# Optimization experiments

Measured on AMD Instinct MI355X. Metric: run time of the kernel, lower is better.

The kernel has to match this reference:

```python
import jax, jax.numpy as jnp
import numpy as np

NUM_PHONEMES = 512
D = 128  # embed_dim == hidden_channels == out_channels (forced by residuals)
N = 50000
E = 500000
PAD_ID = 0
LN_EPS = 1e-5


def setup_inputs() -> dict:
    key = jax.random.key(0)
    ks = jax.random.split(key, 12)
    node_ids = jax.random.randint(ks[0], (N,), 0, NUM_PHONEMES)
    edge_index = jax.random.randint(ks[1], (2, E), 0, N)
    emb = jax.random.normal(ks[2], (NUM_PHONEMES, D), jnp.float32) * 0.05
    emb = emb.at[PAD_ID].set(0.0)  # padding_idx row zeroed
    W1 = jax.random.normal(ks[3], (D, D), jnp.float32) * (1.0 / np.sqrt(D))
    b1 = jnp.zeros((D,), jnp.float32)
    W2 = jax.random.normal(ks[4], (D, D), jnp.float32) * (1.0 / np.sqrt(D))
    b2 = jnp.zeros((D,), jnp.float32)
    g1 = jnp.ones((D,), jnp.float32)
    beta1 = jnp.zeros((D,), jnp.float32)
    g2 = jnp.ones((D,), jnp.float32)
    beta2 = jnp.zeros((D,), jnp.float32)
    return {"node_ids": node_ids, "edge_index": edge_index, "emb": emb,
            "W1": W1, "b1": b1, "W2": W2, "b2": b2,
            "g1": g1, "beta1": beta1, "g2": g2, "beta2": beta2}


def _gcn_conv(x, src, dst, W, b):
    """PyG GCNConv with add_self_loops=True, normalize=True.
    out = D^{-1/2} (A + I) D^{-1/2} (x W) + b, deg computed after self-loops."""
    n = x.shape[0]
    loop = jnp.arange(n, dtype=src.dtype)
    src_f = jnp.concatenate([src, loop])  # [E+N]
    dst_f = jnp.concatenate([dst, loop])
    deg = jax.ops.segment_sum(jnp.ones_like(dst_f, dtype=x.dtype), dst_f,
                              num_segments=n)  # >=1 due to self-loops
    dis = jax.lax.rsqrt(deg)
    norm = dis[src_f] * dis[dst_f]  # [E+N]
    h = x @ W  # [N, D_out]
    msg = h[src_f] * norm[:, None]  # [E+N, D_out] gather (memory-bound)
    out = jax.ops.segment_sum(msg, dst_f, num_segments=n)  # scatter-add
    return out + b


def _layernorm(x, g, b):
    mu = jnp.mean(x, axis=-1, keepdims=True)
    var = jnp.mean(jnp.square(x - mu), axis=-1, keepdims=True)
    return (x - mu) * jax.lax.rsqrt(var + LN_EPS) * g + b


def reference(node_ids, edge_index, emb, W1, b1, W2, b2, g1, beta1, g2, beta2):
    src, dst = edge_index[0], edge_index[1]
    x = emb[node_ids]  # embedding lookup [N, D]
    h1 = _gcn_conv(x, src, dst, W1, b1)
    x = _layernorm(x + h1, g1, beta1)  # dropout is identity in eval mode
    h2 = _gcn_conv(x, src, dst, W2, b2)
    x = _layernorm(x + h2, g2, beta2)
    return x
```

## Files before the change

kernel.cpp:

```cpp
#include <hip/hip_runtime.h>

#define DD 128
#define CAP 32
#define SPILL_MAX 4096

typedef __attribute__((ext_vector_type(8))) short short8;
typedef __attribute__((ext_vector_type(4))) float float4v;

static __device__ __forceinline__ unsigned short f2bf(float x) {
    unsigned u = __builtin_bit_cast(unsigned, x);
    u += 0x7fffu + ((u >> 16) & 1u);
    return (unsigned short)(u >> 16);
}
static __device__ __forceinline__ float bflo(unsigned u) {
    return __builtin_bit_cast(float, u << 16);
}
static __device__ __forceinline__ float bfhi(unsigned u) {
    return __builtin_bit_cast(float, u & 0xffff0000u);
}

__global__ __launch_bounds__(256) void k_init(const float* __restrict__ emb,
                                              const float* __restrict__ W1,
                                              const float* __restrict__ W2,
                                              unsigned* __restrict__ embW1b,
                                              unsigned short* __restrict__ Wb,
                                              const int* __restrict__ src,
                                              const int* __restrict__ dst,
                                              const int* __restrict__ node_ids,
                                              int* __restrict__ cursor,
                                              unsigned* __restrict__ recs,
                                              int* __restrict__ spillCnt,
                                              int* __restrict__ spill_d,
                                              int* __restrict__ spill_r, int E) {
    int blk = blockIdx.x;
    if (blk < 128) {
        int w = threadIdx.x >> 6;
        int t = threadIdx.x & 63;
        int p = blk * 4 + w;
        int c0 = t * 2, c1 = t * 2 + 1;
        float s0 = 0.f, s1 = 0.f;
#pragma unroll 8
        for (int k = 0; k < DD; k++) {
            float e = emb[p * DD + k];
            s0 += e * W1[k * DD + c0];
            s1 += e * W1[k * DD + c1];
        }
        embW1b[p * 64 + t] = (unsigned)f2bf(s0) | ((unsigned)f2bf(s1) << 16);
    } else if (blk < 136) {
        int t = (blk - 128) * 256 + threadIdx.x;
        int nt = t >> 8, ks = (t >> 6) & 3, lane = t & 63;
        int n = nt * 16 + (lane & 15);
        int kbase = ks * 32 + (lane >> 4) * 8;
        unsigned short* o = Wb + (size_t)t * 8;
#pragma unroll
        for (int j = 0; j < 8; j++)
            o[j] = f2bf(W2[(kbase + j) * DD + n]);
    } else {
        int base = ((blk - 136) * 256 + threadIdx.x) * 4;
        if (base >= E) return;
#pragma unroll
        for (int u = 0; u < 4; u++) {
            int e = base + u;
            if (e >= E) break;
            int s = src[e], d = dst[e];
            unsigned rec = (unsigned)s | ((unsigned)node_ids[s] << 16);
            int pos = atomicAdd(&cursor[d], 1);
            if (pos < CAP) {
                recs[(size_t)d * CAP + pos] = rec;
            } else {
                int sp = atomicAdd(spillCnt, 1);
                if (sp < SPILL_MAX) { spill_d[sp] = d; spill_r[sp] = (int)rec; }
            }
        }
    }
}

__global__ __launch_bounds__(256) void k_node1(const int* __restrict__ cursor,
                                               const unsigned* __restrict__ recs,
                                               const int* __restrict__ node_ids,
                                               const float* __restrict__ emb,
                                               const unsigned* __restrict__ embW1b,
                                               const int* __restrict__ spillCnt,
                                               const int* __restrict__ spill_d,
                                               const int* __restrict__ spill_r,
                                               const float* __restrict__ b1,
                                               const float* __restrict__ g1,
                                               const float* __restrict__ beta1,
                                               unsigned* __restrict__ x1b, int N) {
    int gid = blockIdx.x * blockDim.x + threadIdx.x;
    int wave = gid >> 6;
    int lane = threadIdx.x & 63;
    int qtr = lane >> 4;
    int l = lane & 15;
    int qbase = lane & 48;
    int i = wave * 4 + qtr;
    if (i >= N) return;
    int dg = cursor[i];
    int r0 = i * CAP;
    int r1 = r0 + ((dg < CAP) ? dg : CAP);
    int c = l * 8;
    float a0 = 0.f, a1 = 0.f, a2 = 0.f, a3 = 0.f, a4 = 0.f, a5 = 0.f, a6 = 0.f, a7 = 0.f;
    for (int j0 = r0; j0 < r1; j0 += 16) {
        int pidx = j0 + l;
        unsigned rv = recs[(pidx < r1) ? pidx : (r1 - 1)];
        int lim = r1 - j0;
#pragma unroll
        for (int q = 0; q < 16; q++) {
            unsigned rec = __shfl(rv, qbase + q, 64);
            int s = rec & 0xFFFFu;
            float n = rsqrtf((float)cursor[s] + 1.0f);
            n = (q < lim) ? n : 0.f;
            uint4 a = *(const uint4*)(embW1b + ((rec >> 16) & 511u) * 64 + l * 4);
            a0 += bflo(a.x) * n; a1 += bfhi(a.x) * n;
            a2 += bflo(a.y) * n; a3 += bfhi(a.y) * n;
            a4 += bflo(a.z) * n; a5 += bfhi(a.z) * n;
            a6 += bflo(a.w) * n; a7 += bfhi(a.w) * n;
        }
    }
    if (dg > CAP) {
        int sc = *spillCnt; if (sc > SPILL_MAX) sc = SPILL_MAX;
        for (int j = 0; j < sc; j++) {
            if (spill_d[j] == i) {
                unsigned rec = (unsigned)spill_r[j];
                int s = rec & 0xFFFFu;
                float n = rsqrtf((float)cursor[s] + 1.0f);
                uint4 a = *(const uint4*)(embW1b + ((rec >> 16) & 511u) * 64 + l * 4);
                a0 += bflo(a.x) * n; a1 += bfhi(a.x) * n;
                a2 += bflo(a.y) * n; a3 += bfhi(a.y) * n;
                a4 += bflo(a.z) * n; a5 += bfhi(a.z) * n;
                a6 += bflo(a.w) * n; a7 += bfhi(a.w) * n;
            }
        }
    }
    float di = rsqrtf((float)dg + 1.0f);
    int pid = node_ids[i];
    float4 ev0 = *(const float4*)(emb + (size_t)pid * DD + c);
    float4 ev1 = *(const float4*)(emb + (size_t)pid * DD + c + 4);
    uint4 hw = *(const uint4*)(embW1b + pid * 64 + l * 4);
    float4 bb0 = *(const float4*)(b1 + c);
    float4 bb1 = *(const float4*)(b1 + c + 4);
    float v0 = ev0.x + di * (a0 + di * bflo(hw.x)) + bb0.x;
    float v1 = ev0.y + di * (a1 + di * bfhi(hw.x)) + bb0.y;
    float v2 = ev0.z + di * (a2 + di * bflo(hw.y)) + bb0.z;
    float v3 = ev0.w + di * (a3 + di * bfhi(hw.y)) + bb0.w;
    float v4 = ev1.x + di * (a4 + di * bflo(hw.z)) + bb1.x;
    float v5 = ev1.y + di * (a5 + di * bfhi(hw.z)) + bb1.y;
    float v6 = ev1.z + di * (a6 + di * bflo(hw.w)) + bb1.z;
    float v7 = ev1.w + di * (a7 + di * bfhi(hw.w)) + bb1.w;
    float sum = v0 + v1 + v2 + v3 + v4 + v5 + v6 + v7;
#pragma unroll
    for (int o = 8; o >= 1; o >>= 1) sum += __shfl_xor(sum, o, 64);
    float mu = sum * (1.f / DD);
    float d0 = v0 - mu, d1 = v1 - mu, d2 = v2 - mu, d3 = v3 - mu;
    float d4 = v4 - mu, d5 = v5 - mu, d6 = v6 - mu, d7 = v7 - mu;
    float ss = d0 * d0 + d1 * d1 + d2 * d2 + d3 * d3 + d4 * d4 + d5 * d5 + d6 * d6 + d7 * d7;
#pragma unroll
    for (int o = 8; o >= 1; o >>= 1) ss += __shfl_xor(ss, o, 64);
    float r = rsqrtf(ss * (1.f / DD) + 1e-5f);
    float4 gg0 = *(const float4*)(g1 + c);
    float4 gg1 = *(const float4*)(g1 + c + 4);
    float4 be0 = *(const float4*)(beta1 + c);
    float4 be1 = *(const float4*)(beta1 + c + 4);
    float o0 = d0 * r * gg0.x + be0.x;
    float o1 = d1 * r * gg0.y + be0.y;
    float o2 = d2 * r * gg0.z + be0.z;
    float o3 = d3 * r * gg0.w + be0.w;
    float o4 = d4 * r * gg1.x + be1.x;
    float o5 = d5 * r * gg1.y + be1.y;
    float o6 = d6 * r * gg1.z + be1.z;
    float o7 = d7 * r * gg1.w + be1.w;
    uint4 pk;
    pk.x = (unsigned)f2bf(o0) | ((unsigned)f2bf(o1) << 16);
    pk.y = (unsigned)f2bf(o2) | ((unsigned)f2bf(o3) << 16);
    pk.z = (unsigned)f2bf(o4) | ((unsigned)f2bf(o5) << 16);
    pk.w = (unsigned)f2bf(o6) | ((unsigned)f2bf(o7) << 16);
    *(uint4*)(x1b + (size_t)i * 64 + l * 4) = pk;
}

__global__ __launch_bounds__(256) void k_node2(const int* __restrict__ cursor,
                                               const unsigned* __restrict__ recs,
                                               const unsigned* __restrict__ x1b,
                                               const int* __restrict__ spillCnt,
                                               const int* __restrict__ spill_d,
                                               const int* __restrict__ spill_r,
                                               const float* __restrict__ b2,
                                               const float* __restrict__ g2,
                                               const float* __restrict__ beta2,
                                               const unsigned short* __restrict__ Wb,
                                               float* __restrict__ out, int N) {
    __shared__ unsigned tileA[16 * 68];
    __shared__ float tileH[16 * 132];
    int wv = threadIdx.x >> 6;
    int lane = threadIdx.x & 63;
    int qtr = lane >> 4;
    int l = lane & 15;
    int qbase = lane & 48;
    int base16 = blockIdx.x * 16;
    int i = base16 + wv * 4 + qtr;
    uint4 xv = make_uint4(0, 0, 0, 0);
    float bb[8] = {0, 0, 0, 0, 0, 0, 0, 0};
    int c = l * 8;
    if (i < N) {
        int dg = cursor[i];
        int r0 = i * CAP;
        int r1 = r0 + ((dg < CAP) ? dg : CAP);
        float a0 = 0.f, a1 = 0.f, a2 = 0.f, a3 = 0.f, a4 = 0.f, a5 = 0.f, a6 = 0.f, a7 = 0.f;
        for (int j0 = r0; j0 < r1; j0 += 16) {
            int pidx = j0 + l;
            unsigned rv = recs[(pidx < r1) ? pidx : (r1 - 1)];
            int lim = r1 - j0;
#pragma unroll
            for (int q = 0; q < 16; q++) {
                unsigned s = __shfl(rv, qbase + q, 64) & 0xFFFFu;
                float n = rsqrtf((float)cursor[s] + 1.0f);
                n = (q < lim) ? n : 0.f;
                uint4 a = *(const uint4*)(x1b + (size_t)s * 64 + l * 4);
                a0 += bflo(a.x) * n; a1 += bfhi(a.x) * n;
                a2 += bflo(a.y) * n; a3 += bfhi(a.y) * n;
                a4 += bflo(a.z) * n; a5 += bfhi(a.z) * n;
                a6 += bflo(a.w) * n; a7 += bfhi(a.w) * n;
            }
        }
        if (dg > CAP) {
            int sc = *spillCnt; if (sc > SPILL_MAX) sc = SPILL_MAX;
            for (int j = 0; j < sc; j++) {
                if (spill_d[j] == i) {
                    unsigned s = (unsigned)spill_r[j] & 0xFFFFu;
                    float n = rsqrtf((float)cursor[s] + 1.0f);
                    uint4 a = *(const uint4*)(x1b + (size_t)s * 64 + l * 4);
                    a0 += bflo(a.x) * n; a1 += bfhi(a.x) * n;
                    a2 += bflo(a.y) * n; a3 += bfhi(a.y) * n;
                    a4 += bflo(a.z) * n; a5 += bfhi(a.z) * n;
                    a6 += bflo(a.w) * n; a7 += bfhi(a.w) * n;
                }
            }
        }
        float di = rsqrtf((float)dg + 1.0f);
        xv = *(const uint4*)(x1b + (size_t)i * 64 + l * 4);
        float z0 = a0 + di * bflo(xv.x);
        float z1 = a1 + di * bfhi(xv.x);
        float z2 = a2 + di * bflo(xv.y);
        float z3 = a3 + di * bfhi(xv.y);
        float z4 = a4 + di * bflo(xv.z);
        float z5 = a5 + di * bfhi(xv.z);
        float z6 = a6 + di * bflo(xv.w);
        float z7 = a7 + di * bfhi(xv.w);
        uint4 pk;
        pk.x = (unsigned)f2bf(z0) | ((unsigned)f2bf(z1) << 16);
        pk.y = (unsigned)f2bf(z2) | ((unsigned)f2bf(z3) << 16);
        pk.z = (unsigned)f2bf(z4) | ((unsigned)f2bf(z5) << 16);
        pk.w = (unsigned)f2bf(z6) | ((unsigned)f2bf(z7) << 16);
        *(uint4*)(tileA + (wv * 4 + qtr) * 68 + l * 4) = pk;
        float4 t0 = *(const float4*)(b2 + c);
        float4 t1 = *(const float4*)(b2 + c + 4);
        bb[0] = t0.x; bb[1] = t0.y; bb[2] = t0.z; bb[3] = t0.w;
        bb[4] = t1.x; bb[5] = t1.y; bb[6] = t1.z; bb[7] = t1.w;
    }
    __syncthreads();
    {
        int m = l;
        int quad = qtr;
        short8 afr[4];
        const char* tb = (const char*)tileA;
#pragma unroll
        for (int ks = 0; ks < 4; ks++)
            afr[ks] = *(const short8*)(tb + m * 272 + ks * 64 + quad * 16);
        float dr[4];
        {
            int rb = base16 + quad * 4;
            const int4 cv = *(const int4*)(cursor + rb);
            dr[0] = rsqrtf((float)cv.x + 1.f);
            dr[1] = rsqrtf((float)cv.y + 1.f);
            dr[2] = rsqrtf((float)cv.z + 1.f);
            dr[3] = rsqrtf((float)cv.w + 1.f);
        }
        const short8* bp = (const short8*)Wb;
#pragma unroll
        for (int t = 0; t < 2; t++) {
            int nt = wv * 2 + t;
            float4v acc = {0.f, 0.f, 0.f, 0.f};
#pragma unroll
            for (int ks = 0; ks < 4; ks++) {
                short8 bfr = bp[(nt * 4 + ks) * 64 + lane];
                acc = __builtin_amdgcn_mfma_f32_16x16x32_bf16(afr[ks], bfr, acc, 0, 0, 0);
            }
            int col = nt * 16 + m;
#pragma unroll
            for (int r = 0; r < 4; r++)
                tileH[(quad * 4 + r) * 132 + col] = acc[r] * dr[r];
        }
    }
    __syncthreads();
    if (i >= N) return;
    int row_local = wv * 4 + qtr;
    float4 h0 = *(const float4*)(tileH + row_local * 132 + c);
    float4 h1 = *(const float4*)(tileH + row_local * 132 + c + 4);
    float v0 = bflo(xv.x) + h0.x + bb[0];
    float v1 = bfhi(xv.x) + h0.y + bb[1];
    float v2 = bflo(xv.y) + h0.z + bb[2];
    float v3 = bfhi(xv.y) + h0.w + bb[3];
    float v4 = bflo(xv.z) + h1.x + bb[4];
    float v5 = bfhi(xv.z) + h1.y + bb[5];
    float v6 = bflo(xv.w) + h1.z + bb[6];
    float v7 = bfhi(xv.w) + h1.w + bb[7];
    float sum = v0 + v1 + v2 + v3 + v4 + v5 + v6 + v7;
#pragma unroll
    for (int o = 8; o >= 1; o >>= 1) sum += __shfl_xor(sum, o, 64);
    float mu = sum * (1.f / DD);
    float d0 = v0 - mu, d1 = v1 - mu, d2 = v2 - mu, d3 = v3 - mu;
    float d4 = v4 - mu, d5 = v5 - mu, d6 = v6 - mu, d7 = v7 - mu;
    float ss = d0 * d0 + d1 * d1 + d2 * d2 + d3 * d3 + d4 * d4 + d5 * d5 + d6 * d6 + d7 * d7;
#pragma unroll
    for (int o = 8; o >= 1; o >>= 1) ss += __shfl_xor(ss, o, 64);
    float r = rsqrtf(ss * (1.f / DD) + 1e-5f);
    float4 gg0 = *(const float4*)(g2 + c);
    float4 gg1 = *(const float4*)(g2 + c + 4);
    float4 be0 = *(const float4*)(beta2 + c);
    float4 be1 = *(const float4*)(beta2 + c + 4);
    float4 o0, o1;
    o0.x = d0 * r * gg0.x + be0.x;
    o0.y = d1 * r * gg0.y + be0.y;
    o0.z = d2 * r * gg0.z + be0.z;
    o0.w = d3 * r * gg0.w + be0.w;
    o1.x = d4 * r * gg1.x + be1.x;
    o1.y = d5 * r * gg1.y + be1.y;
    o1.z = d6 * r * gg1.z + be1.z;
    o1.w = d7 * r * gg1.w + be1.w;
    *(float4*)(out + (size_t)i * DD + c) = o0;
    *(float4*)(out + (size_t)i * DD + c + 4) = o1;
}

extern "C" void kernel_launch(void* const* d_in, const int* in_sizes, int n_in,
                              void* d_out, int out_size, void* d_ws, size_t ws_size,
                              hipStream_t stream) {
    const int* node_ids = (const int*)d_in[0];
    const int* edge_index = (const int*)d_in[1];
    const float* emb   = (const float*)d_in[2];
    const float* W1    = (const float*)d_in[3];
    const float* b1    = (const float*)d_in[4];
    const float* W2    = (const float*)d_in[5];
    const float* b2    = (const float*)d_in[6];
    const float* g1    = (const float*)d_in[7];
    const float* beta1 = (const float*)d_in[8];
    const float* g2    = (const float*)d_in[9];
    const float* beta2 = (const float*)d_in[10];
    const int N = in_sizes[0];
    const int E = in_sizes[1] / 2;
    const int* srcp = edge_index;
    const int* dstp = edge_index + E;
    float* out = (float*)d_out;

    char* base = (char*)d_ws;
    size_t off = 0;
    auto carve = [&](size_t bytes) -> void* {
        void* p = base + off;
        off += (bytes + 255) & ~(size_t)255;
        return p;
    };
    int*      meta   = (int*)carve((size_t)(N + 17) * 4);
    int*      cursor = meta;
    int*      spillCnt = meta + N + 16;
    int*      spill_d = (int*)carve((size_t)SPILL_MAX * 4);
    int*      spill_r = (int*)carve((size_t)SPILL_MAX * 4);
    unsigned* recs   = (unsigned*)carve((size_t)N * CAP * 4);
    unsigned* embW1b = (unsigned*)carve((size_t)512 * 64 * 4);
    unsigned* x1b    = (unsigned*)carve((size_t)(N + 16) * 64 * 4);
    unsigned short* Wb = (unsigned short*)carve((size_t)DD * DD * 2);
    (void)ws_size; (void)n_in; (void)out_size;

    const int TB = 256;
    const int Hb = (E + 1023) / 1024;

    hipMemsetAsync(meta, 0, (size_t)(N + 17) * 4, stream);
    k_init<<<136 + Hb, TB, 0, stream>>>(emb, W1, W2, embW1b, Wb,
                                        srcp, dstp, node_ids, cursor, recs,
                                        spillCnt, spill_d, spill_r, E);

    long long tn = (long long)((N + 3) / 4) * 64;
    int nodeBlocks = (int)((tn + TB - 1) / TB);
    k_node1<<<nodeBlocks, TB, 0, stream>>>(cursor, recs, node_ids, emb, embW1b,
                                           spillCnt, spill_d, spill_r,
                                           b1, g1, beta1, x1b, N);
    int blocks16 = (N + 15) / 16;
    k_node2<<<blocks16, TB, 0, stream>>>(cursor, recs, x1b,
                                         spillCnt, spill_d, spill_r,
                                         b2, g2, beta2, Wb, out, N);
}
```

Measured before the change: 192.9 us.

## Batch neighbor gathers, precompute inverse-sqrt degrees, give each wave its own MFMA tile

```diff
diff --git a/kernel.cpp b/kernel.cpp
--- a/kernel.cpp
+++ b/kernel.cpp
@@ -86,7 +86,8 @@
                                                const float* __restrict__ b1,
                                                const float* __restrict__ g1,
                                                const float* __restrict__ beta1,
-                                               unsigned* __restrict__ x1b, int N) {
+                                               unsigned* __restrict__ x1b,
+                                               float* __restrict__ disf, int N) {
     int gid = blockIdx.x * blockDim.x + threadIdx.x;
     int wave = gid >> 6;
     int lane = threadIdx.x & 63;
@@ -96,21 +97,27 @@
     int i = wave * 4 + qtr;
     if (i >= N) return;
     int dg = cursor[i];
-    int r0 = i * CAP;
-    int r1 = r0 + ((dg < CAP) ? dg : CAP);
+    int dgc = (dg < CAP) ? dg : CAP;
+    unsigned rv0 = recs[(size_t)i * CAP + l];
+    unsigned rv1 = recs[(size_t)i * CAP + 16 + l];
     int c = l * 8;
     float a0 = 0.f, a1 = 0.f, a2 = 0.f, a3 = 0.f, a4 = 0.f, a5 = 0.f, a6 = 0.f, a7 = 0.f;
-    for (int j0 = r0; j0 < r1; j0 += 16) {
-        int pidx = j0 + l;
-        unsigned rv = recs[(pidx < r1) ? pidx : (r1 - 1)];
-        int lim = r1 - j0;
-#pragma unroll
-        for (int q = 0; q < 16; q++) {
-            unsigned rec = __shfl(rv, qbase + q, 64);
-            int s = rec & 0xFFFFu;
-            float n = rsqrtf((float)cursor[s] + 1.0f);
-            n = (q < lim) ? n : 0.f;
-            uint4 a = *(const uint4*)(embW1b + ((rec >> 16) & 511u) * 64 + l * 4);
+    for (int j0 = 0; j0 < dgc; j0 += 8) {
+        unsigned rvs = (j0 < 16) ? rv0 : rv1;
+        uint4 buf[8]; int cb[8]; float nn[8];
+#pragma unroll
+        for (int q = 0; q < 8; q++) {
+            int e = j0 + q;
+            int ec = (e < dgc) ? e : (dgc - 1);
+            unsigned rec = __shfl(rvs, qbase + (ec & 15), 64);
+            nn[q] = (e < dgc) ? 1.f : 0.f;
+            buf[q] = *(const uint4*)(embW1b + ((rec >> 16) & 511u) * 64 + l * 4);
+            cb[q] = cursor[rec & 0xFFFFu];
+        }
+#pragma unroll
+        for (int q = 0; q < 8; q++) {
+            float n = rsqrtf((float)cb[q] + 1.f) * nn[q];
+            uint4 a = buf[q];
             a0 += bflo(a.x) * n; a1 += bfhi(a.x) * n;
             a2 += bflo(a.y) * n; a3 += bfhi(a.y) * n;
             a4 += bflo(a.z) * n; a5 += bfhi(a.z) * n;
@@ -175,11 +182,13 @@
     pk.z = (unsigned)f2bf(o4) | ((unsigned)f2bf(o5) << 16);
     pk.w = (unsigned)f2bf(o6) | ((unsigned)f2bf(o7) << 16);
     *(uint4*)(x1b + (size_t)i * 64 + l * 4) = pk;
+    if (l == 0) disf[i] = di;
 }
 
 __global__ __launch_bounds__(256) void k_node2(const int* __restrict__ cursor,
                                                const unsigned* __restrict__ recs,
                                                const unsigned* __restrict__ x1b,
+                                               const float* __restrict__ disf,
                                                const int* __restrict__ spillCnt,
                                                const int* __restrict__ spill_d,
                                                const int* __restrict__ spill_r,
@@ -188,146 +197,127 @@
                                                const float* __restrict__ beta2,
                                                const unsigned short* __restrict__ Wb,
                                                float* __restrict__ out, int N) {
-    __shared__ unsigned tileA[16 * 68];
-    __shared__ float tileH[16 * 132];
+    __shared__ unsigned tileA[4][16 * 68];
     int wv = threadIdx.x >> 6;
     int lane = threadIdx.x & 63;
     int qtr = lane >> 4;
     int l = lane & 15;
     int qbase = lane & 48;
-    int base16 = blockIdx.x * 16;
-    int i = base16 + wv * 4 + qtr;
-    uint4 xv = make_uint4(0, 0, 0, 0);
-    float bb[8] = {0, 0, 0, 0, 0, 0, 0, 0};
-    int c = l * 8;
-    if (i < N) {
-        int dg = cursor[i];
-        int r0 = i * CAP;
-        int r1 = r0 + ((dg < CAP) ? dg : CAP);
-        float a0 = 0.f, a1 = 0.f, a2 = 0.f, a3 = 0.f, a4 = 0.f, a5 = 0.f, a6 = 0.f, a7 = 0.f;
-        for (int j0 = r0; j0 < r1; j0 += 16) {
-            int pidx = j0 + l;
-            unsigned rv = recs[(pidx < r1) ? pidx : (r1 - 1)];
-            int lim = r1 - j0;
-#pragma unroll
-            for (int q = 0; q < 16; q++) {
-                unsigned s = __shfl(rv, qbase + q, 64) & 0xFFFFu;
-                float n = rsqrtf((float)cursor[s] + 1.0f);
-                n = (q < lim) ? n : 0.f;
-                uint4 a = *(const uint4*)(x1b + (size_t)s * 64 + l * 4);
-                a0 += bflo(a.x) * n; a1 += bfhi(a.x) * n;
-                a2 += bflo(a.y) * n; a3 += bfhi(a.y) * n;
-                a4 += bflo(a.z) * n; a5 += bfhi(a.z) * n;
-                a6 += bflo(a.w) * n; a7 += bfhi(a.w) * n;
-            }
-        }
-        if (dg > CAP) {
-            int sc = *spillCnt; if (sc > SPILL_MAX) sc = SPILL_MAX;
-            for (int j = 0; j < sc; j++) {
-                if (spill_d[j] == i) {
-                    unsigned s = (unsigned)spill_r[j] & 0xFFFFu;
-                    float n = rsqrtf((float)cursor[s] + 1.0f);
-                    uint4 a = *(const uint4*)(x1b + (size_t)s * 64 + l * 4);
+    int wbase = (blockIdx.x * 4 + wv) * 16;
+    unsigned* myT = &tileA[wv][0];
+#pragma unroll 1
+    for (int k = 0; k < 4; k++) {
+        int rr = k * 4 + qtr;
+        int i = wbase + rr;
+        uint4 pk = make_uint4(0, 0, 0, 0);
+        if (i < N) {
+            int dg = cursor[i];
+            int dgc = (dg < CAP) ? dg : CAP;
+            unsigned rv0 = recs[(size_t)i * CAP + l];
+            unsigned rv1 = recs[(size_t)i * CAP + 16 + l];
+            float a0 = 0.f, a1 = 0.f, a2 = 0.f, a3 = 0.f, a4 = 0.f, a5 = 0.f, a6 = 0.f, a7 = 0.f;
+            for (int j0 = 0; j0 < dgc; j0 += 8) {
+                unsigned rvs = (j0 < 16) ? rv0 : rv1;
+                uint4 buf[8]; float fb[8]; float nn[8];
+#pragma unroll
+                for (int q = 0; q < 8; q++) {
+                    int e = j0 + q;
+                    int ec = (e < dgc) ? e : (dgc - 1);
+                    unsigned rec = __shfl(rvs, qbase + (ec & 15), 64);
+                    unsigned s = rec & 0xFFFFu;
+                    nn[q] = (e < dgc) ? 1.f : 0.f;
+                    buf[q] = *(const uint4*)(x1b + (size_t)s * 64 + l * 4);
+                    fb[q] = disf[s];
+                }
+#pragma unroll
+                for (int q = 0; q < 8; q++) {
+                    float n = fb[q] * nn[q];
+                    uint4 a = buf[q];
                     a0 += bflo(a.x) * n; a1 += bfhi(a.x) * n;
                     a2 += bflo(a.y) * n; a3 += bfhi(a.y) * n;
                     a4 += bflo(a.z) * n; a5 += bfhi(a.z) * n;
                     a6 += bflo(a.w) * n; a7 += bfhi(a.w) * n;
                 }
             }
-        }
-        float di = rsqrtf((float)dg + 1.0f);
-        xv = *(const uint4*)(x1b + (size_t)i * 64 + l * 4);
-        float z0 = a0 + di * bflo(xv.x);
-        float z1 = a1 + di * bfhi(xv.x);
-        float z2 = a2 + di * bflo(xv.y);
-        float z3 = a3 + di * bfhi(xv.y);
-        float z4 = a4 + di * bflo(xv.z);
-        float z5 = a5 + di * bfhi(xv.z);
-        float z6 = a6 + di * bflo(xv.w);
-        float z7 = a7 + di * bfhi(xv.w);
-        uint4 pk;
-        pk.x = (unsigned)f2bf(z0) | ((unsigned)f2bf(z1) << 16);
-        pk.y = (unsigned)f2bf(z2) | ((unsigned)f2bf(z3) << 16);
-        pk.z = (unsigned)f2bf(z4) | ((unsigned)f2bf(z5) << 16);
-        pk.w = (unsigned)f2bf(z6) | ((unsigned)f2bf(z7) << 16);
-        *(uint4*)(tileA + (wv * 4 + qtr) * 68 + l * 4) = pk;
-        float4 t0 = *(const float4*)(b2 + c);
-        float4 t1 = *(const float4*)(b2 + c + 4);
-        bb[0] = t0.x; bb[1] = t0.y; bb[2] = t0.z; bb[3] = t0.w;
-        bb[4] = t1.x; bb[5] = t1.y; bb[6] = t1.z; bb[7] = t1.w;
+            if (dg > CAP) {
+                int sc = *spillCnt; if (sc > SPILL_MAX) sc = SPILL_MAX;
+                for (int j = 0; j < sc; j++) {
+                    if (spill_d[j] == i) {
+                        unsigned s = (unsigned)spill_r[j] & 0xFFFFu;
+                        float n = disf[s];
+                        uint4 a = *(const uint4*)(x1b + (size_t)s * 64 + l * 4);
+                        a0 += bflo(a.x) * n; a1 += bfhi(a.x) * n;
+                        a2 += bflo(a.y) * n; a3 += bfhi(a.y) * n;
+                        a4 += bflo(a.z) * n; a5 += bfhi(a.z) * n;
+                        a6 += bflo(a.w) * n; a7 += bfhi(a.w) * n;
+                    }
+                }
+            }
+            float di = disf[i];
+            uint4 xv = *(const uint4*)(x1b + (size_t)i * 64 + l * 4);
+            float z0 = a0 + di * bflo(xv.x);
+            float z1 = a1 + di * bfhi(xv.x);
+            float z2 = a2 + di * bflo(xv.y);
+            float z3 = a3 + di * bfhi(xv.y);
+            float z4 = a4 + di * bflo(xv.z);
+            float z5 = a5 + di * bfhi(xv.z);
+            float z6 = a6 + di * bflo(xv.w);
+            float z7 = a7 + di * bfhi(xv.w);
+            pk.x = (unsigned)f2bf(z0) | ((unsigned)f2bf(z1) << 16);
+            pk.y = (unsigned)f2bf(z2) | ((unsigned)f2bf(z3) << 16);
+            pk.z = (unsigned)f2bf(z4) | ((unsigned)f2bf(z5) << 16);
+            pk.w = (unsigned)f2bf(z6) | ((unsigned)f2bf(z7) << 16);
+        }
+        *(uint4*)(myT + rr * 68 + l * 4) = pk;
     }
     __syncthreads();
+    short8 afr[4];
+    const char* tb = (const char*)myT;
+#pragma unroll
+    for (int ks = 0; ks < 4; ks++)
+        afr[ks] = *(const short8*)(tb + l * 272 + ks * 64 + qtr * 16);
+    const short8* bp = (const short8*)Wb;
+    float4v acc[8];
+#pragma unroll
+    for (int nt = 0; nt < 8; nt++) {
+        float4v a = {0.f, 0.f, 0.f, 0.f};
+#pragma unroll
+        for (int ks = 0; ks < 4; ks++)
+            a = __builtin_amdgcn_mfma_f32_16x16x32_bf16(afr[ks], bp[(nt * 4 + ks) * 64 + lane], a, 0, 0, 0);
+        acc[nt] = a;
+    }
+    float dvarr[4];
     {
-        int m = l;
-        int quad = qtr;
-        short8 afr[4];
-        const char* tb = (const char*)tileA;
-#pragma unroll
-        for (int ks = 0; ks < 4; ks++)
-            afr[ks] = *(const short8*)(tb + m * 272 + ks * 64 + quad * 16);
-        float dr[4];
-        {
-            int rb = base16 + quad * 4;
-            const int4 cv = *(const int4*)(cursor + rb);
-            dr[0] = rsqrtf((float)cv.x + 1.f);
-            dr[1] = rsqrtf((float)cv.y + 1.f);
-            dr[2] = rsqrtf((float)cv.z + 1.f);
-            dr[3] = rsqrtf((float)cv.w + 1.f);
-        }
-        const short8* bp = (const short8*)Wb;
-#pragma unroll
-        for (int t = 0; t < 2; t++) {
-            int nt = wv * 2 + t;
-            float4v acc = {0.f, 0.f, 0.f, 0.f};
-#pragma unroll
-            for (int ks = 0; ks < 4; ks++) {
-                short8 bfr = bp[(nt * 4 + ks) * 64 + lane];
-                acc = __builtin_amdgcn_mfma_f32_16x16x32_bf16(afr[ks], bfr, acc, 0, 0, 0);
-            }
-            int col = nt * 16 + m;
-#pragma unroll
-            for (int r = 0; r < 4; r++)
-                tileH[(quad * 4 + r) * 132 + col] = acc[r] * dr[r];
-        }
-    }
-    __syncthreads();
-    if (i >= N) return;
-    int row_local = wv * 4 + qtr;
-    float4 h0 = *(const float4*)(tileH + row_local * 132 + c);
-    float4 h1 = *(const float4*)(tileH + row_local * 132 + c + 4);
-    float v0 = bflo(xv.x) + h0.x + bb[0];
-    float v1 = bfhi(xv.x) + h0.y + bb[1];
-    float v2 = bflo(xv.y) + h0.z + bb[2];
-    float v3 = bfhi(xv.y) + h0.w + bb[3];
-    float v4 = bflo(xv.z) + h1.x + bb[4];
-    float v5 = bfhi(xv.z) + h1.y + bb[5];
-    float v6 = bflo(xv.w) + h1.z + bb[6];
-    float v7 = bfhi(xv.w) + h1.w + bb[7];
-    float sum = v0 + v1 + v2 + v3 + v4 + v5 + v6 + v7;
-#pragma unroll
-    for (int o = 8; o >= 1; o >>= 1) sum += __shfl_xor(sum, o, 64);
-    float mu = sum * (1.f / DD);
-    float d0 = v0 - mu, d1 = v1 - mu, d2 = v2 - mu, d3 = v3 - mu;
-    float d4 = v4 - mu, d5 = v5 - mu, d6 = v6 - mu, d7 = v7 - mu;
-    float ss = d0 * d0 + d1 * d1 + d2 * d2 + d3 * d3 + d4 * d4 + d5 * d5 + d6 * d6 + d7 * d7;
-#pragma unroll
-    for (int o = 8; o >= 1; o >>= 1) ss += __shfl_xor(ss, o, 64);
-    float r = rsqrtf(ss * (1.f / DD) + 1e-5f);
-    float4 gg0 = *(const float4*)(g2 + c);
-    float4 gg1 = *(const float4*)(g2 + c + 4);
-    float4 be0 = *(const float4*)(beta2 + c);
-    float4 be1 = *(const float4*)(beta2 + c + 4);
-    float4 o0, o1;
-    o0.x = d0 * r * gg0.x + be0.x;
-    o0.y = d1 * r * gg0.y + be0.y;
-    o0.z = d2 * r * gg0.z + be0.z;
-    o0.w = d3 * r * gg0.w + be0.w;
-    o1.x = d4 * r * gg1.x + be1.x;
-    o1.y = d5 * r * gg1.y + be1.y;
-    o1.z = d6 * r * gg1.z + be1.z;
-    o1.w = d7 * r * gg1.w + be1.w;
-    *(float4*)(out + (size_t)i * DD + c) = o0;
-    *(float4*)(out + (size_t)i * DD + c + 4) = o1;
+        float4 dv4 = *(const float4*)(disf + wbase + qtr * 4);
+        dvarr[0] = dv4.x; dvarr[1] = dv4.y; dvarr[2] = dv4.z; dvarr[3] = dv4.w;
+    }
+#pragma unroll
+    for (int r = 0; r < 4; r++) {
+        int rowg = wbase + qtr * 4 + r;
+        if (rowg < N) {
+            float di = dvarr[r];
+            float vv[8]; float sum = 0.f;
+#pragma unroll
+            for (int nt = 0; nt < 8; nt++) {
+                unsigned xw = x1b[(size_t)rowg * 64 + nt * 8 + (l >> 1)];
+                float xr = (l & 1) ? bfhi(xw) : bflo(xw);
+                vv[nt] = xr + di * acc[nt][r] + b2[nt * 16 + l];
+                sum += vv[nt];
+            }
+#pragma unroll
+            for (int o = 8; o >= 1; o >>= 1) sum += __shfl_xor(sum, o, 64);
+            float mu = sum * (1.f / DD);
+            float ss = 0.f;
+#pragma unroll
+            for (int nt = 0; nt < 8; nt++) { float d = vv[nt] - mu; vv[nt] = d; ss += d * d; }
+#pragma unroll
+            for (int o = 8; o >= 1; o >>= 1) ss += __shfl_xor(ss, o, 64);
+            float rstd = rsqrtf(ss * (1.f / DD) + 1e-5f);
+#pragma unroll
+            for (int nt = 0; nt < 8; nt++)
+                out[(size_t)rowg * DD + nt * 16 + l] = vv[nt] * rstd * g2[nt * 16 + l] + beta2[nt * 16 + l];
+        }
+    }
 }
 
 extern "C" void kernel_launch(void* const* d_in, const int* in_sizes, int n_in,
@@ -364,7 +354,8 @@
     int*      spill_r = (int*)carve((size_t)SPILL_MAX * 4);
     unsigned* recs   = (unsigned*)carve((size_t)N * CAP * 4);
     unsigned* embW1b = (unsigned*)carve((size_t)512 * 64 * 4);
-    unsigned* x1b    = (unsigned*)carve((size_t)(N + 16) * 64 * 4);
+    unsigned* x1b    = (unsigned*)carve((size_t)(N + 64) * 64 * 4);
+    float*    disf   = (float*)carve((size_t)(N + 64) * 4);
     unsigned short* Wb = (unsigned short*)carve((size_t)DD * DD * 2);
     (void)ws_size; (void)n_in; (void)out_size;
 
@@ -380,9 +371,9 @@
     int nodeBlocks = (int)((tn + TB - 1) / TB);
     k_node1<<<nodeBlocks, TB, 0, stream>>>(cursor, recs, node_ids, emb, embW1b,
                                            spillCnt, spill_d, spill_r,
-                                           b1, g1, beta1, x1b, N);
-    int blocks16 = (N + 15) / 16;
-    k_node2<<<blocks16, TB, 0, stream>>>(cursor, recs, x1b,
+                                           b1, g1, beta1, x1b, disf, N);
+    int blocks64 = (N + 63) / 64;
+    k_node2<<<blocks64, TB, 0, stream>>>(cursor, recs, x1b, disf,
                                          spillCnt, spill_d, spill_r,
                                          b2, g2, beta2, Wb, out, N);
 }
```

After: 167.8 us. 1.15x faster.
